# Optimization experiments

Hardware: AMD Instinct MI355X
Metric: run time of the kernel (lower is better)

Reference implementation:

```python
import jax, jax.numpy as jnp
import numpy as np

N = 100000   # nodes
E = 1000000  # directed edges
D = 64       # in_dim
H = 64       # hid_dim
O = 64       # out_dim


def _lin_init(key, fan_in, fan_out):
    # torch nn.Linear default init: U(-1/sqrt(fan_in), 1/sqrt(fan_in))
    k1, k2 = jax.random.split(key)
    s = 1.0 / np.sqrt(fan_in)
    W = jax.random.uniform(k1, (fan_in, fan_out), jnp.float32, -s, s)
    b = jax.random.uniform(k2, (fan_out,), jnp.float32, -s, s)
    return W, b


def setup_inputs() -> dict:
    key = jax.random.key(0)
    ks = jax.random.split(key, 6)
    x = jax.random.normal(ks[0], (N, D), jnp.float32)
    src = jax.random.randint(ks[1], (E,), 0, N)
    dst = jax.random.randint(ks[2], (E,), 0, N)
    W1, b1 = _lin_init(ks[3], 2 * D, H)
    W2, b2 = _lin_init(ks[4], 2 * H, H)
    W3, b3 = _lin_init(ks[5], 2 * H, O)
    return {"x": x, "src": src, "dst": dst,
            "W1": W1, "b1": b1, "W2": W2, "b2": b2, "W3": W3, "b3": b3}


def _graphconv_left(x, s, d, n):
    # DGL GraphConv(norm='left', weight=False, bias=False):
    # divide src features by src out-degree (clamped min 1), sum at dst.
    deg = jax.ops.segment_sum(jnp.ones_like(s, x.dtype), s, num_segments=n)
    deg = jnp.maximum(deg, 1.0)
    msg = (x / deg[:, None])[s]                       # [E, F] gather
    return jax.ops.segment_sum(msg, d, num_segments=n)  # [N, F] scatter-add


def _sage_layer(x, s, d, n, W, b, use_activation):
    agg = _graphconv_left(x, s, d, n)
    h = jnp.concatenate([x, agg], axis=1) @ W + b
    return jax.nn.relu(h) if use_activation else h


def reference(x, src, dst, W1, b1, W2, b2, W3, b3):
    n = x.shape[0]
    # dir_seq = 'OIU': out-edges, reversed edges, undirected (both directions)
    usrc = jnp.concatenate([src, dst])
    udst = jnp.concatenate([dst, src])
    x = _sage_layer(x, src, dst, n, W1, b1, True)    # 'O'
    x = _sage_layer(x, dst, src, n, W2, b2, True)    # 'I' (reverse graph)
    x = _sage_layer(x, usrc, udst, n, W3, b3, False) # 'U' (undirected)
    return x
```

## Files before the change

kernel.cpp:

```cpp
#include <hip/hip_runtime.h>
#include <hip/hip_fp16.h>


#define BSHIFT 10
#define BMASK  ((1 << BSHIFT) - 1)
#define NBMAX  128
#define PCHUNK 2048
#define HCHUNK 4096

__global__ __launch_bounds__(256) void bucket_hist_k(
    const int* __restrict__ src, const int* __restrict__ dst,
    int* __restrict__ bcnt_out, int* __restrict__ bcnt_in, int E) {
    __shared__ int h0[NBMAX], h1[NBMAX];
    const int t = threadIdx.x;
    const int e0 = blockIdx.x * HCHUNK;
    int n = E - e0; if (n > HCHUNK) n = HCHUNK;
    for (int i = t; i < NBMAX; i += 256) { h0[i] = 0; h1[i] = 0; }
    __syncthreads();
    for (int i = t; i < n; i += 256) {
        atomicAdd(&h0[src[e0 + i] >> BSHIFT], 1);
        atomicAdd(&h1[dst[e0 + i] >> BSHIFT], 1);
    }
    __syncthreads();
    if (t < NBMAX) {
        int c = h0[t];
        if (c) atomicAdd(&bcnt_out[t], c);
    } else {
        int b = t - NBMAX;
        int c = h1[b];
        if (c) atomicAdd(&bcnt_in[b], c);
    }
}

__global__ void finalize_r_k(const int* __restrict__ deg_out, const int* __restrict__ deg_in,
                             float* __restrict__ r_out, float* __restrict__ r_in,
                             float* __restrict__ r_und, int N) {
    int t = blockIdx.x * blockDim.x + threadIdx.x;
    if (t < N) {
        int a = deg_out[t], b = deg_in[t];
        r_out[t] = 1.0f / (float)(a < 1 ? 1 : a);
        r_in[t]  = 1.0f / (float)(b < 1 ? 1 : b);
        int c = a + b;
        r_und[t] = 1.0f / (float)(c < 1 ? 1 : c);
    }
}

__global__ void bucket_scan_k(const int* __restrict__ bcnt_out, const int* __restrict__ bcnt_in,
                              int* __restrict__ bip_out, int* __restrict__ bip_in,
                              int* __restrict__ bcur_out, int* __restrict__ bcur_in, int NB) {
    __shared__ int s[1024];
    int t = threadIdx.x;
#pragma unroll 1
    for (int pass = 0; pass < 2; ++pass) {
        const int* bcnt = pass ? bcnt_in : bcnt_out;
        int* bip = pass ? bip_in : bip_out;
        int* bcur = pass ? bcur_in : bcur_out;
        int v = (t < NB) ? bcnt[t] : 0;
        s[t] = v; __syncthreads();
        for (int off = 1; off < 1024; off <<= 1) {
            int x = (t >= off) ? s[t - off] : 0;
            __syncthreads();
            s[t] += x;
            __syncthreads();
        }
        int excl = s[t] - v;
        if (t < NB) { bip[t] = excl; bcur[t] = excl; }
        if (t == NB) bip[NB] = excl;
        __syncthreads();
    }
}

__global__ __launch_bounds__(256) void partition_k(
    const int* __restrict__ src, const int* __restrict__ dst,
    int* __restrict__ bcur_out, int* __restrict__ bcur_in,
    unsigned* __restrict__ part_out, unsigned* __restrict__ part_in, int E) {
    __shared__ int sS[PCHUNK], sD[PCHUNK];
    __shared__ int hist[2][NBMAX];
    __shared__ int gbase[2][NBMAX];
    const int t = threadIdx.x;
    const int e0 = blockIdx.x * PCHUNK;
    int n = E - e0; if (n > PCHUNK) n = PCHUNK;

    for (int i = t; i < NBMAX; i += 256) { hist[0][i] = 0; hist[1][i] = 0; }
    __syncthreads();
    for (int i = t; i < n; i += 256) {
        int s = src[e0 + i], d = dst[e0 + i];
        sS[i] = s; sD[i] = d;
        atomicAdd(&hist[0][d >> BSHIFT], 1);
        atomicAdd(&hist[1][s >> BSHIFT], 1);
    }
    __syncthreads();
    if (t < NBMAX) {
        int c = hist[0][t];
        gbase[0][t] = c ? atomicAdd(&bcur_in[t], c) : 0;
        hist[0][t] = 0;
    } else {
        int b = t - NBMAX;
        int c = hist[1][b];
        gbase[1][b] = c ? atomicAdd(&bcur_out[b], c) : 0;
        hist[1][b] = 0;
    }
    __syncthreads();
    for (int i = t; i < n; i += 256) {
        int s = sS[i], d = sD[i];
        int bi = d >> BSHIFT;
        int p = gbase[0][bi] + atomicAdd(&hist[0][bi], 1);
        part_in[p] = ((unsigned)s << BSHIFT) | (unsigned)(d & BMASK);
        int bo = s >> BSHIFT;
        int q = gbase[1][bo] + atomicAdd(&hist[1][bo], 1);
        part_out[q] = ((unsigned)d << BSHIFT) | (unsigned)(s & BMASK);
    }
}

__global__ __launch_bounds__(256) void bucket_sort_k(
    const unsigned* __restrict__ pa, const int* __restrict__ bipa,
    const unsigned* __restrict__ pb, const int* __restrict__ bipb,
    int* __restrict__ ipa, int* __restrict__ ipb,
    int* __restrict__ cola, int* __restrict__ colb,
    int* __restrict__ dega, int* __restrict__ degb, int N, int E) {
    const unsigned* part = blockIdx.y ? pb : pa;
    const int* bip = blockIdx.y ? bipb : bipa;
    int* ip  = blockIdx.y ? ipb : ipa;
    int* col = blockIdx.y ? colb : cola;
    int* deg = blockIdx.y ? degb : dega;
    __shared__ int cnt[1024];
    __shared__ int ps[256];
    const int g = blockIdx.x, t = threadIdx.x;
    const int b = bip[g], e = bip[g + 1];

    for (int i = t; i < 1024; i += 256) cnt[i] = 0;
    __syncthreads();
    for (int i = b + t; i < e; i += 256) atomicAdd(&cnt[part[i] & (unsigned)BMASK], 1);
    __syncthreads();

    int c0 = cnt[4 * t + 0], c1 = cnt[4 * t + 1], c2 = cnt[4 * t + 2], c3 = cnt[4 * t + 3];
    int tot = c0 + c1 + c2 + c3;
    ps[t] = tot;
    __syncthreads();
    for (int off = 1; off < 256; off <<= 1) {
        int v = (t >= off) ? ps[t - off] : 0;
        __syncthreads();
        ps[t] += v;
        __syncthreads();
    }
    int base = b + ps[t] - tot;
    int node0 = (g << BSHIFT) + 4 * t;
    int cc[4] = {c0, c1, c2, c3};
#pragma unroll
    for (int j = 0; j < 4; ++j) {
        cnt[4 * t + j] = base;
        int node = node0 + j;
        if (node < N) { ip[node] = base; deg[node] = cc[j]; }
        base += cc[j];
    }
    if (g == 0 && t == 0) ip[N] = E;
    __syncthreads();
    for (int i = b + t; i < e; i += 256) {
        unsigned rec = part[i];
        int p = atomicAdd(&cnt[rec & (unsigned)BMASK], 1);
        col[p] = (int)(rec >> BSHIFT);
    }
}

__global__ void scale_rows_k(const float* __restrict__ in, const float* __restrict__ r,
                             __half* __restrict__ out, int n4) {
    int t = blockIdx.x * blockDim.x + threadIdx.x;
    if (t < n4) {
        float s = r[t >> 4];
        float4 v = ((const float4*)in)[t];
        __half2 p01 = __floats2half2_rn(v.x * s, v.y * s);
        __half2 p23 = __floats2half2_rn(v.z * s, v.w * s);
        uint2 u;
        u.x = *(unsigned*)&p01;
        u.y = *(unsigned*)&p23;
        *(uint2*)(out + ((size_t)t << 2)) = u;
    }
}

__device__ __forceinline__ void acc_row(float4& acc, uint2 u) {
    __half2 h01 = *(__half2*)&u.x, h23 = *(__half2*)&u.y;
    acc.x += __low2float(h01); acc.y += __high2float(h01);
    acc.z += __low2float(h23); acc.w += __high2float(h23);
}

__device__ __forceinline__ void agg_list(const __half* __restrict__ hs,
                                         const int* __restrict__ col,
                                         int b, int e, int lane, int grp, int fo,
                                         float4& a0, float4& a1, float4& a2, float4& a3) {
    for (int base = b; base < e; base += 64) {
        int cnt = e - base; if (cnt > 64) cnt = 64;
        int my = (lane < cnt) ? col[base + lane] : 0;
        for (int j = 0; j < cnt; j += 16) {
            int i0 = j + grp, i1 = j + 4 + grp, i2 = j + 8 + grp, i3 = j + 12 + grp;
            int n0 = __shfl(my, i0 < cnt ? i0 : 0);
            int n1 = __shfl(my, i1 < cnt ? i1 : 0);
            int n2 = __shfl(my, i2 < cnt ? i2 : 0);
            int n3 = __shfl(my, i3 < cnt ? i3 : 0);
            uint2 u0 = *(const uint2*)(hs + ((size_t)n0 << 6) + (fo << 2));
            uint2 u1 = *(const uint2*)(hs + ((size_t)n1 << 6) + (fo << 2));
            uint2 u2 = *(const uint2*)(hs + ((size_t)n2 << 6) + (fo << 2));
            uint2 u3 = *(const uint2*)(hs + ((size_t)n3 << 6) + (fo << 2));
            if (i0 < cnt) acc_row(a0, u0);
            if (i1 < cnt) acc_row(a1, u1);
            if (i2 < cnt) acc_row(a2, u2);
            if (i3 < cnt) acc_row(a3, u3);
        }
    }
}

__device__ __forceinline__ void agg_finish(float4 a0, float4 a1, float4 a2, float4 a3,
                                           float* __restrict__ agg, int node,
                                           int lane, int fo) {
    float4 acc;
    acc.x = (a0.x + a1.x) + (a2.x + a3.x);
    acc.y = (a0.y + a1.y) + (a2.y + a3.y);
    acc.z = (a0.z + a1.z) + (a2.z + a3.z);
    acc.w = (a0.w + a1.w) + (a2.w + a3.w);
    acc.x += __shfl_xor(acc.x, 16); acc.y += __shfl_xor(acc.y, 16);
    acc.z += __shfl_xor(acc.z, 16); acc.w += __shfl_xor(acc.w, 16);
    acc.x += __shfl_xor(acc.x, 32); acc.y += __shfl_xor(acc.y, 32);
    acc.z += __shfl_xor(acc.z, 32); acc.w += __shfl_xor(acc.w, 32);
    if (lane < 16) ((float4*)(agg + ((size_t)node << 6)))[fo] = acc;
}

__global__ void agg_k(const __half* __restrict__ hs, const int* __restrict__ ip,
                      const int* __restrict__ col, float* __restrict__ agg, int N) {
    int node = (blockIdx.x * blockDim.x + threadIdx.x) >> 6;
    int lane = threadIdx.x & 63;
    if (node >= N) return;
    const int grp = lane >> 4, fo = lane & 15;
    float4 z = make_float4(0.f, 0.f, 0.f, 0.f);
    float4 a0 = z, a1 = z, a2 = z, a3 = z;
    agg_list(hs, col, ip[node], ip[node + 1], lane, grp, fo, a0, a1, a2, a3);
    agg_finish(a0, a1, a2, a3, agg, node, lane, fo);
}

__global__ void agg_dual_k(const __half* __restrict__ hs,
                           const int* __restrict__ ipA, const int* __restrict__ colA,
                           const int* __restrict__ ipB, const int* __restrict__ colB,
                           float* __restrict__ agg, int N) {
    int node = (blockIdx.x * blockDim.x + threadIdx.x) >> 6;
    int lane = threadIdx.x & 63;
    if (node >= N) return;
    const int grp = lane >> 4, fo = lane & 15;
    float4 z = make_float4(0.f, 0.f, 0.f, 0.f);
    float4 a0 = z, a1 = z, a2 = z, a3 = z;
    agg_list(hs, colA, ipA[node], ipA[node + 1], lane, grp, fo, a0, a1, a2, a3);
    agg_list(hs, colB, ipB[node], ipB[node + 1], lane, grp, fo, a0, a1, a2, a3);
    agg_finish(a0, a1, a2, a3, agg, node, lane, fo);
}

template <bool RELU, bool WRITE_HS>
__global__ __launch_bounds__(256, 2) void gemm_cat_k(
    const float* X, const float* A,
    const float* __restrict__ W, const float* __restrict__ B,
    const float* __restrict__ rs, __half* __restrict__ hs_out,
    float* out, int N) {
    __shared__ float sW[128 * 64];
    __shared__ float sX[64 * 64];
    __shared__ float sA[64 * 64];
    const int tid = threadIdx.x;

    for (int i = tid; i < 2048; i += 256) ((float4*)sW)[i] = ((const float4*)W)[i];

    const int row0 = blockIdx.x * 64;
    for (int i = tid; i < 1024; i += 256) {
        int r = i >> 4, c4 = (i & 15) << 2;
        int gr = row0 + r;
        float4 xv = make_float4(0.f, 0.f, 0.f, 0.f), av = xv;
        if (gr < N) {
            xv = ((const float4*)X)[(size_t)gr * 16 + (i & 15)];
            av = ((const float4*)A)[(size_t)gr * 16 + (i & 15)];
        }
        int sc = c4 ^ ((r & 12) << 1);
        *(float4*)&sX[(r << 6) + sc] = xv;
        *(float4*)&sA[(r << 6) + sc] = av;
    }
    __syncthreads();

    const int c0 = (tid & 15) << 2;
    const int r0 = (tid >> 4) << 2;
    const int sw = (r0 & 12) << 1;

    float4 bv = *(const float4*)(B + c0);
    float acc[4][4];
#pragma unroll
    for (int i = 0; i < 4; ++i) {
        acc[i][0] = bv.x; acc[i][1] = bv.y; acc[i][2] = bv.z; acc[i][3] = bv.w;
    }

#define GEMM_ROW(i, av)                                                       \
    acc[i][0] = fmaf(av.x, w0.x, acc[i][0]); acc[i][1] = fmaf(av.x, w0.y, acc[i][1]); \
    acc[i][2] = fmaf(av.x, w0.z, acc[i][2]); acc[i][3] = fmaf(av.x, w0.w, acc[i][3]); \
    acc[i][0] = fmaf(av.y, w1.x, acc[i][0]); acc[i][1] = fmaf(av.y, w1.y, acc[i][1]); \
    acc[i][2] = fmaf(av.y, w1.z, acc[i][2]); acc[i][3] = fmaf(av.y, w1.w, acc[i][3]); \
    acc[i][0] = fmaf(av.z, w2.x, acc[i][0]); acc[i][1] = fmaf(av.z, w2.y, acc[i][1]); \
    acc[i][2] = fmaf(av.z, w2.z, acc[i][2]); acc[i][3] = fmaf(av.z, w2.w, acc[i][3]); \
    acc[i][0] = fmaf(av.w, w3.x, acc[i][0]); acc[i][1] = fmaf(av.w, w3.y, acc[i][1]); \
    acc[i][2] = fmaf(av.w, w3.z, acc[i][2]); acc[i][3] = fmaf(av.w, w3.w, acc[i][3]);

#pragma unroll 4
    for (int kb = 0; kb < 64; kb += 4) {
        const int kx = kb ^ sw;
        float4 w0 = *(const float4*)&sW[((kb + 0) << 6) + c0];
        float4 w1 = *(const float4*)&sW[((kb + 1) << 6) + c0];
        float4 w2 = *(const float4*)&sW[((kb + 2) << 6) + c0];
        float4 w3 = *(const float4*)&sW[((kb + 3) << 6) + c0];
        float4 a0 = *(const float4*)&sX[((r0 + 0) << 6) + kx];
        float4 a1 = *(const float4*)&sX[((r0 + 1) << 6) + kx];
        float4 a2 = *(const float4*)&sX[((r0 + 2) << 6) + kx];
        float4 a3 = *(const float4*)&sX[((r0 + 3) << 6) + kx];
        GEMM_ROW(0, a0) GEMM_ROW(1, a1) GEMM_ROW(2, a2) GEMM_ROW(3, a3)
    }
#pragma unroll 4
    for (int kb = 0; kb < 64; kb += 4) {
        const int kx = kb ^ sw;
        float4 w0 = *(const float4*)&sW[((kb + 64) << 6) + c0];
        float4 w1 = *(const float4*)&sW[((kb + 65) << 6) + c0];
        float4 w2 = *(const float4*)&sW[((kb + 66) << 6) + c0];
        float4 w3 = *(const float4*)&sW[((kb + 67) << 6) + c0];
        float4 a0 = *(const float4*)&sA[((r0 + 0) << 6) + kx];
        float4 a1 = *(const float4*)&sA[((r0 + 1) << 6) + kx];
        float4 a2 = *(const float4*)&sA[((r0 + 2) << 6) + kx];
        float4 a3 = *(const float4*)&sA[((r0 + 3) << 6) + kx];
        GEMM_ROW(0, a0) GEMM_ROW(1, a1) GEMM_ROW(2, a2) GEMM_ROW(3, a3)
    }
#undef GEMM_ROW

#pragma unroll
    for (int i = 0; i < 4; ++i) {
        int gr = row0 + r0 + i;
        if (gr < N) {
            float4 o;
            o.x = RELU ? fmaxf(acc[i][0], 0.f) : acc[i][0];
            o.y = RELU ? fmaxf(acc[i][1], 0.f) : acc[i][1];
            o.z = RELU ? fmaxf(acc[i][2], 0.f) : acc[i][2];
            o.w = RELU ? fmaxf(acc[i][3], 0.f) : acc[i][3];
            *(float4*)(out + ((size_t)gr << 6) + c0) = o;
            if (WRITE_HS) {
                float rr = rs[gr];
                __half2 p01 = __floats2half2_rn(o.x * rr, o.y * rr);
                __half2 p23 = __floats2half2_rn(o.z * rr, o.w * rr);
                uint2 u;
                u.x = *(unsigned*)&p01;
                u.y = *(unsigned*)&p23;
                *(uint2*)(hs_out + ((size_t)gr << 6) + c0) = u;
            }
        }
    }
}

extern "C" void kernel_launch(void* const* d_in, const int* in_sizes, int n_in,
                              void* d_out, int out_size, void* d_ws, size_t ws_size,
                              hipStream_t stream) {
    const float* x  = (const float*)d_in[0];
    const int* src  = (const int*)d_in[1];
    const int* dst  = (const int*)d_in[2];
    const float* W1 = (const float*)d_in[3];
    const float* b1 = (const float*)d_in[4];
    const float* W2 = (const float*)d_in[5];
    const float* b2 = (const float*)d_in[6];
    const float* W3 = (const float*)d_in[7];
    const float* b3 = (const float*)d_in[8];

    const int N = in_sizes[0] / 64;
    const int E = in_sizes[1];
    const int NB = (N + BMASK) >> BSHIFT;

    float* bufH  = (float*)d_ws;
    __half* bufHS = (__half*)(bufH + (size_t)N * 64);
    int* deg_out = (int*)(bufHS + (size_t)N * 64);
    int* deg_in  = deg_out + N;
    float* r_out = (float*)(deg_in + N);
    float* r_in  = r_out + N;
    float* r_und = r_in + N;
    int* ip_out  = (int*)(r_und + N);
    int* ip_in   = ip_out + (N + 1);
    int* bcnt_out = ip_in + (N + 1);
    int* bcnt_in  = bcnt_out + NB;
    int* bip_out  = bcnt_in + NB;
    int* bip_in   = bip_out + (NB + 1);
    int* bcur_out = bip_in + (NB + 1);
    int* bcur_in  = bcur_out + NB;
    unsigned* part_out = (unsigned*)(bcur_in + NB);
    unsigned* part_in  = part_out + E;
    int* col_out = (int*)(part_in + E);
    int* col_in  = col_out + E;

    float* aggB = (float*)d_out;

    const int TPB = 256;
    const int gN  = (N + TPB - 1) / TPB;
    const int n4  = N * 16;
    const int g4  = (n4 + TPB - 1) / TPB;
    const int gAg = (int)(((size_t)N * 64 + TPB - 1) / TPB);
    const int gGm = (N + 63) / 64;
    const int gP  = (E + PCHUNK - 1) / PCHUNK;
    const int gH  = (E + HCHUNK - 1) / HCHUNK;

    hipMemsetAsync(bcnt_out, 0, 2 * (size_t)NB * sizeof(int), stream);
    bucket_hist_k<<<gH, TPB, 0, stream>>>(src, dst, bcnt_out, bcnt_in, E);
    bucket_scan_k<<<1, 1024, 0, stream>>>(bcnt_out, bcnt_in, bip_out, bip_in,
                                          bcur_out, bcur_in, NB);
    partition_k<<<gP, TPB, 0, stream>>>(src, dst, bcur_out, bcur_in,
                                        part_out, part_in, E);
    bucket_sort_k<<<dim3(NB, 2), TPB, 0, stream>>>(part_out, bip_out, part_in, bip_in,
                                                   ip_out, ip_in, col_out, col_in,
                                                   deg_out, deg_in, N, E);
    finalize_r_k<<<gN, TPB, 0, stream>>>(deg_out, deg_in, r_out, r_in, r_und, N);

    scale_rows_k<<<g4, TPB, 0, stream>>>(x, r_out, bufHS, n4);
    agg_k<<<gAg, TPB, 0, stream>>>(bufHS, ip_in, col_in, aggB, N);
    gemm_cat_k<true, true><<<gGm, TPB, 0, stream>>>(x, aggB, W1, b1, r_in, bufHS, bufH, N);

    agg_k<<<gAg, TPB, 0, stream>>>(bufHS, ip_out, col_out, aggB, N);
    gemm_cat_k<true, true><<<gGm, TPB, 0, stream>>>(bufH, aggB, W2, b2, r_und, bufHS, bufH, N);

    agg_dual_k<<<gAg, TPB, 0, stream>>>(bufHS, ip_in, col_in, ip_out, col_out, aggB, N);
    gemm_cat_k<false, false><<<gGm, TPB, 0, stream>>>(bufH, aggB, W3, b3, nullptr, nullptr,
                                                      (float*)d_out, N);
}
```

Baseline: 304.4 us.

## Drop reciprocal-degree kernel, fold into consumers; 1024-thread bucket sort; pre-shifted columns

Removes the finalize_r_k launch and its three reciprocal arrays by computing 1/deg inline in scale_rows_k and in the GEMM epilogue. The undirected degree is formed there from deg_in plus deg_out. bucket_sort_k now runs 1024 threads per bucket, one node per thread, in place of 4 nodes per thread. Column indices are stored as byte offsets (node<<7), so the aggregation gathers skip the index shift. This saves a launch and some memory traffic, at the cost of a longer 1024-wide scan with more barriers. The byte offsets also cap the node index near 2^24, which is fine for N=100k.

```diff
diff --git a/kernel.cpp b/kernel.cpp
--- a/kernel.cpp
+++ b/kernel.cpp
@@ -29,19 +29,6 @@
         int b = t - NBMAX;
         int c = h1[b];
         if (c) atomicAdd(&bcnt_in[b], c);
-    }
-}
-
-__global__ void finalize_r_k(const int* __restrict__ deg_out, const int* __restrict__ deg_in,
-                             float* __restrict__ r_out, float* __restrict__ r_in,
-                             float* __restrict__ r_und, int N) {
-    int t = blockIdx.x * blockDim.x + threadIdx.x;
-    if (t < N) {
-        int a = deg_out[t], b = deg_in[t];
-        r_out[t] = 1.0f / (float)(a < 1 ? 1 : a);
-        r_in[t]  = 1.0f / (float)(b < 1 ? 1 : b);
-        int c = a + b;
-        r_und[t] = 1.0f / (float)(c < 1 ? 1 : c);
     }
 }
 
@@ -112,7 +99,7 @@
     }
 }
 
-__global__ __launch_bounds__(256) void bucket_sort_k(
+__global__ __launch_bounds__(1024) void bucket_sort_k(
     const unsigned* __restrict__ pa, const int* __restrict__ bipa,
     const unsigned* __restrict__ pb, const int* __restrict__ bipb,
     int* __restrict__ ipa, int* __restrict__ ipb,
@@ -124,49 +111,43 @@
     int* col = blockIdx.y ? colb : cola;
     int* deg = blockIdx.y ? degb : dega;
     __shared__ int cnt[1024];
-    __shared__ int ps[256];
+    __shared__ int s[1024];
     const int g = blockIdx.x, t = threadIdx.x;
     const int b = bip[g], e = bip[g + 1];
 
-    for (int i = t; i < 1024; i += 256) cnt[i] = 0;
-    __syncthreads();
-    for (int i = b + t; i < e; i += 256) atomicAdd(&cnt[part[i] & (unsigned)BMASK], 1);
-    __syncthreads();
-
-    int c0 = cnt[4 * t + 0], c1 = cnt[4 * t + 1], c2 = cnt[4 * t + 2], c3 = cnt[4 * t + 3];
-    int tot = c0 + c1 + c2 + c3;
-    ps[t] = tot;
-    __syncthreads();
-    for (int off = 1; off < 256; off <<= 1) {
-        int v = (t >= off) ? ps[t - off] : 0;
+    cnt[t] = 0;
+    __syncthreads();
+    for (int i = b + t; i < e; i += 1024) atomicAdd(&cnt[part[i] & (unsigned)BMASK], 1);
+    __syncthreads();
+
+    int v = cnt[t];
+    s[t] = v;
+    __syncthreads();
+    for (int off = 1; off < 1024; off <<= 1) {
+        int x = (t >= off) ? s[t - off] : 0;
         __syncthreads();
-        ps[t] += v;
+        s[t] += x;
         __syncthreads();
     }
-    int base = b + ps[t] - tot;
-    int node0 = (g << BSHIFT) + 4 * t;
-    int cc[4] = {c0, c1, c2, c3};
-#pragma unroll
-    for (int j = 0; j < 4; ++j) {
-        cnt[4 * t + j] = base;
-        int node = node0 + j;
-        if (node < N) { ip[node] = base; deg[node] = cc[j]; }
-        base += cc[j];
-    }
+    int base = b + s[t] - v;
+    int node = (g << BSHIFT) + t;
+    if (node < N) { ip[node] = base; deg[node] = v; }
+    cnt[t] = base;
     if (g == 0 && t == 0) ip[N] = E;
     __syncthreads();
-    for (int i = b + t; i < e; i += 256) {
+    for (int i = b + t; i < e; i += 1024) {
         unsigned rec = part[i];
         int p = atomicAdd(&cnt[rec & (unsigned)BMASK], 1);
-        col[p] = (int)(rec >> BSHIFT);
-    }
-}
-
-__global__ void scale_rows_k(const float* __restrict__ in, const float* __restrict__ r,
+        col[p] = (int)((rec >> BSHIFT) << 7);
+    }
+}
+
+__global__ void scale_rows_k(const float* __restrict__ in, const int* __restrict__ deg,
                              __half* __restrict__ out, int n4) {
     int t = blockIdx.x * blockDim.x + threadIdx.x;
     if (t < n4) {
-        float s = r[t >> 4];
+        int m = deg[t >> 4];
+        float s = 1.0f / (float)(m < 1 ? 1 : m);
         float4 v = ((const float4*)in)[t];
         __half2 p01 = __floats2half2_rn(v.x * s, v.y * s);
         __half2 p23 = __floats2half2_rn(v.z * s, v.w * s);
@@ -183,23 +164,23 @@
     acc.z += __low2float(h23); acc.w += __high2float(h23);
 }
 
-__device__ __forceinline__ void agg_list(const __half* __restrict__ hs,
+__device__ __forceinline__ void agg_list(const char* __restrict__ hsb,
                                          const int* __restrict__ col,
-                                         int b, int e, int lane, int grp, int fo,
+                                         int b, int e, int lane, int grp, int fo8,
                                          float4& a0, float4& a1, float4& a2, float4& a3) {
     for (int base = b; base < e; base += 64) {
         int cnt = e - base; if (cnt > 64) cnt = 64;
         int my = (lane < cnt) ? col[base + lane] : 0;
         for (int j = 0; j < cnt; j += 16) {
             int i0 = j + grp, i1 = j + 4 + grp, i2 = j + 8 + grp, i3 = j + 12 + grp;
-            int n0 = __shfl(my, i0 < cnt ? i0 : 0);
-            int n1 = __shfl(my, i1 < cnt ? i1 : 0);
-            int n2 = __shfl(my, i2 < cnt ? i2 : 0);
-            int n3 = __shfl(my, i3 < cnt ? i3 : 0);
-            uint2 u0 = *(const uint2*)(hs + ((size_t)n0 << 6) + (fo << 2));
-            uint2 u1 = *(const uint2*)(hs + ((size_t)n1 << 6) + (fo << 2));
-            uint2 u2 = *(const uint2*)(hs + ((size_t)n2 << 6) + (fo << 2));
-            uint2 u3 = *(const uint2*)(hs + ((size_t)n3 << 6) + (fo << 2));
+            int o0 = __shfl(my, i0 < cnt ? i0 : 0);
+            int o1 = __shfl(my, i1 < cnt ? i1 : 0);
+            int o2 = __shfl(my, i2 < cnt ? i2 : 0);
+            int o3 = __shfl(my, i3 < cnt ? i3 : 0);
+            uint2 u0 = *(const uint2*)(hsb + o0 + fo8);
+            uint2 u1 = *(const uint2*)(hsb + o1 + fo8);
+            uint2 u2 = *(const uint2*)(hsb + o2 + fo8);
+            uint2 u3 = *(const uint2*)(hsb + o3 + fo8);
             if (i0 < cnt) acc_row(a0, u0);
             if (i1 < cnt) acc_row(a1, u1);
             if (i2 < cnt) acc_row(a2, u2);
@@ -228,10 +209,10 @@
     int node = (blockIdx.x * blockDim.x + threadIdx.x) >> 6;
     int lane = threadIdx.x & 63;
     if (node >= N) return;
-    const int grp = lane >> 4, fo = lane & 15;
+    const int grp = lane >> 4, fo = lane & 15, fo8 = fo << 3;
     float4 z = make_float4(0.f, 0.f, 0.f, 0.f);
     float4 a0 = z, a1 = z, a2 = z, a3 = z;
-    agg_list(hs, col, ip[node], ip[node + 1], lane, grp, fo, a0, a1, a2, a3);
+    agg_list((const char*)hs, col, ip[node], ip[node + 1], lane, grp, fo8, a0, a1, a2, a3);
     agg_finish(a0, a1, a2, a3, agg, node, lane, fo);
 }
 
@@ -242,20 +223,20 @@
     int node = (blockIdx.x * blockDim.x + threadIdx.x) >> 6;
     int lane = threadIdx.x & 63;
     if (node >= N) return;
-    const int grp = lane >> 4, fo = lane & 15;
+    const int grp = lane >> 4, fo = lane & 15, fo8 = fo << 3;
     float4 z = make_float4(0.f, 0.f, 0.f, 0.f);
     float4 a0 = z, a1 = z, a2 = z, a3 = z;
-    agg_list(hs, colA, ipA[node], ipA[node + 1], lane, grp, fo, a0, a1, a2, a3);
-    agg_list(hs, colB, ipB[node], ipB[node + 1], lane, grp, fo, a0, a1, a2, a3);
+    agg_list((const char*)hs, colA, ipA[node], ipA[node + 1], lane, grp, fo8, a0, a1, a2, a3);
+    agg_list((const char*)hs, colB, ipB[node], ipB[node + 1], lane, grp, fo8, a0, a1, a2, a3);
     agg_finish(a0, a1, a2, a3, agg, node, lane, fo);
 }
 
-template <bool RELU, bool WRITE_HS>
+template <bool RELU, bool WRITE_HS, bool DEG2>
 __global__ __launch_bounds__(256, 2) void gemm_cat_k(
     const float* X, const float* A,
     const float* __restrict__ W, const float* __restrict__ B,
-    const float* __restrict__ rs, __half* __restrict__ hs_out,
-    float* out, int N) {
+    const int* __restrict__ dga, const int* __restrict__ dgb,
+    __half* __restrict__ hs_out, float* out, int N) {
     __shared__ float sW[128 * 64];
     __shared__ float sX[64 * 64];
     __shared__ float sA[64 * 64];
@@ -338,7 +319,8 @@
             o.w = RELU ? fmaxf(acc[i][3], 0.f) : acc[i][3];
             *(float4*)(out + ((size_t)gr << 6) + c0) = o;
             if (WRITE_HS) {
-                float rr = rs[gr];
+                int m = dga[gr] + (DEG2 ? dgb[gr] : 0);
+                float rr = 1.0f / (float)(m < 1 ? 1 : m);
                 __half2 p01 = __floats2half2_rn(o.x * rr, o.y * rr);
                 __half2 p23 = __floats2half2_rn(o.z * rr, o.w * rr);
                 uint2 u;
@@ -371,10 +353,7 @@
     __half* bufHS = (__half*)(bufH + (size_t)N * 64);
     int* deg_out = (int*)(bufHS + (size_t)N * 64);
     int* deg_in  = deg_out + N;
-    float* r_out = (float*)(deg_in + N);
-    float* r_in  = r_out + N;
-    float* r_und = r_in + N;
-    int* ip_out  = (int*)(r_und + N);
+    int* ip_out  = deg_in + N;
     int* ip_in   = ip_out + (N + 1);
     int* bcnt_out = ip_in + (N + 1);
     int* bcnt_in  = bcnt_out + NB;
@@ -390,7 +369,6 @@
     float* aggB = (float*)d_out;
 
     const int TPB = 256;
-    const int gN  = (N + TPB - 1) / TPB;
     const int n4  = N * 16;
     const int g4  = (n4 + TPB - 1) / TPB;
     const int gAg = (int)(((size_t)N * 64 + TPB - 1) / TPB);
@@ -404,19 +382,21 @@
                                           bcur_out, bcur_in, NB);
     partition_k<<<gP, TPB, 0, stream>>>(src, dst, bcur_out, bcur_in,
                                         part_out, part_in, E);
-    bucket_sort_k<<<dim3(NB, 2), TPB, 0, stream>>>(part_out, bip_out, part_in, bip_in,
-                                                   ip_out, ip_in, col_out, col_in,
-                                                   deg_out, deg_in, N, E);
-    finalize_r_k<<<gN, TPB, 0, stream>>>(deg_out, deg_in, r_out, r_in, r_und, N);
-
-    scale_rows_k<<<g4, TPB, 0, stream>>>(x, r_out, bufHS, n4);
+    bucket_sort_k<<<dim3(NB, 2), 1024, 0, stream>>>(part_out, bip_out, part_in, bip_in,
+                                                    ip_out, ip_in, col_out, col_in,
+                                                    deg_out, deg_in, N, E);
+
+    scale_rows_k<<<g4, TPB, 0, stream>>>(x, deg_out, bufHS, n4);
     agg_k<<<gAg, TPB, 0, stream>>>(bufHS, ip_in, col_in, aggB, N);
-    gemm_cat_k<true, true><<<gGm, TPB, 0, stream>>>(x, aggB, W1, b1, r_in, bufHS, bufH, N);
+    gemm_cat_k<true, true, false><<<gGm, TPB, 0, stream>>>(x, aggB, W1, b1,
+                                                           deg_in, nullptr, bufHS, bufH, N);
 
     agg_k<<<gAg, TPB, 0, stream>>>(bufHS, ip_out, col_out, aggB, N);
-    gemm_cat_k<true, true><<<gGm, TPB, 0, stream>>>(bufH, aggB, W2, b2, r_und, bufHS, bufH, N);
+    gemm_cat_k<true, true, true><<<gGm, TPB, 0, stream>>>(bufH, aggB, W2, b2,
+                                                          deg_in, deg_out, bufHS, bufH, N);
 
     agg_dual_k<<<gAg, TPB, 0, stream>>>(bufHS, ip_in, col_in, ip_out, col_out, aggB, N);
-    gemm_cat_k<false, false><<<gGm, TPB, 0, stream>>>(bufH, aggB, W3, b3, nullptr, nullptr,
-                                                      (float*)d_out, N);
-}
+    gemm_cat_k<false, false, false><<<gGm, TPB, 0, stream>>>(bufH, aggB, W3, b3,
+                                                             nullptr, nullptr, nullptr,
+                                                             (float*)d_out, N);
+}
```

Result: faster. 293.9 us (-3.4%).
